# Kernel tuning notes

Measured on AMD Instinct MI355X. Metric: run time of the kernel, lower is better.

The kernel has to match this reference:

```python
import jax, jax.numpy as jnp
import numpy as np
from jax import lax

GS = 29          # grid_size
DW = 15          # displacement_width
DR = 0.4         # disp_range
N = GS ** 3      # 24389 control points
P = DW ** 2      # 225 in-plane displacements
WIN = (1, 1, 3, 3, 1)
ONE = (1, 1, 1, 1, 1)


def _axis(n):
    # align_corners=False pixel-center coords in [-1, 1], as torch affine_grid
    return (2.0 * jnp.arange(n, dtype=jnp.float32) + 1.0) / n - 1.0


def make_grids():
    a = _axis(GS)
    zc, yc, xc = jnp.meshgrid(a, a, a, indexing='ij')
    grid_xyz = jnp.stack([xc, yc, zc], -1).reshape(-1, 3)  # (N,3) xyz, d-major flatten
    s = DR * _axis(DW)
    A, B = jnp.meshgrid(s, s, indexing='ij')
    Z = jnp.zeros_like(A)
    sx = jnp.stack([B, A, Z], -1).reshape(-1, 3)  # z=0 plane: (s[w], s[h], 0)
    sy = jnp.stack([B, Z, A], -1).reshape(-1, 3)  # y=0 plane: (s[w], 0, s[d])
    sz = jnp.stack([Z, B, A], -1).reshape(-1, 3)  # x=0 plane: (0, s[h], s[d])
    shift_2d = jnp.stack([sx, sy, sz], axis=1)    # (P,3,3): [disp, plane, xyz]
    return grid_xyz, shift_2d


def trilerp(vol, coords, border):
    # vol (C,D,H,W); coords (...,3) normalized xyz; align_corners=False trilinear
    C, D, H, W = vol.shape
    vflat = vol.reshape(C, -1)
    x, y, z = coords[..., 0], coords[..., 1], coords[..., 2]
    ix = 0.5 * ((x + 1.0) * W - 1.0)
    iy = 0.5 * ((y + 1.0) * H - 1.0)
    iz = 0.5 * ((z + 1.0) * D - 1.0)
    x0 = jnp.floor(ix); y0 = jnp.floor(iy); z0 = jnp.floor(iz)
    fx, fy, fz = ix - x0, iy - y0, iz - z0
    x0 = x0.astype(jnp.int32); y0 = y0.astype(jnp.int32); z0 = z0.astype(jnp.int32)
    out = 0.0
    for dz in (0, 1):
        wz = fz if dz else 1.0 - fz
        zi = z0 + dz
        for dy in (0, 1):
            wy = fy if dy else 1.0 - fy
            yi = y0 + dy
            for dx in (0, 1):
                wx = fx if dx else 1.0 - fx
                xi = x0 + dx
                w = wx * wy * wz
                xc = jnp.clip(xi, 0, W - 1)
                yc = jnp.clip(yi, 0, H - 1)
                zc = jnp.clip(zi, 0, D - 1)
                if not border:  # padding_mode='zeros'
                    inb = ((xi >= 0) & (xi < W) & (yi >= 0) & (yi < H) & (zi >= 0) & (zi < D))
                    w = w * inb.astype(vol.dtype)
                idx = (zc * H + yc) * W + xc
                out = out + vflat[:, idx] * w
    return out  # (C, *coords.shape[:-1])


def pad_dh(x):
    # ReplicationPad3d((0,0,2,2,2,2)) on a 5D tensor: pad dims 2 and 3 by 2
    return jnp.pad(x, ((0, 0), (0, 0), (2, 2), (2, 2), (0, 0)), mode='edge')


def minpool(x):
    # -MaxPool3d((3,3,1))(-x)
    return -lax.reduce_window(-x, -jnp.inf, lax.max, WIN, ONE, 'VALID')


def avgpool(x):
    # AvgPool3d((3,3,1), stride=1)
    return lax.reduce_window(x, 0.0, lax.add, WIN, ONE, 'VALID') / 9.0


def grid_smooth(cost):
    # (1,N,DW,DW,3) -> two 3x3 avg passes over the 29^3 control grid (d,h axes)
    cp = cost.transpose(2, 3, 4, 0, 1).reshape(1, 3 * P, GS, GS, GS)
    cp = avgpool(avgpool(pad_dh(cp)))
    return cp.transpose(0, 2, 3, 4, 1).reshape(1, N, DW, DW, 3)


def setup_inputs() -> dict:
    key = jax.random.key(0)
    k1, k2 = jax.random.split(key)
    C, V = 8, 64
    feat00 = jax.random.normal(k1, (1, C, V, V, V), jnp.float32)
    feat50 = jax.random.normal(k2, (1, C, V, V, V), jnp.float32)
    grid_xyz, shift_2d = make_grids()
    shift_2d_min = jnp.array(jnp.broadcast_to(shift_2d[None, None], (1, N, P, 3, 3)))
    alpha = jnp.array([1.0, 0.1, 1.0, 1.0, 0.1, 5.0], jnp.float32)
    return {"feat00": feat00, "feat50": feat50, "shift_2d_min": shift_2d_min,
            "grid_xyz": grid_xyz, "shift_2d": shift_2d, "alpha": alpha}


def reference(feat00, feat50, shift_2d_min, grid_xyz, shift_2d, alpha):
    grid29 = grid_xyz.reshape(GS, GS * GS, 3)
    sm = shift_2d_min.reshape(GS, GS * GS, P, 3, 3)
    f00, f50 = feat00[0], feat50[0]

    def chunk(args):
        g, s = args                                                # (841,3), (841,P,3,3)
        mov = trilerp(f50, g[:, None, None, :] + s, border=True)   # (C,841,P,3)
        fix = trilerp(f00, g, border=False)                        # (C,841)
        ssd = jnp.sum((fix[:, :, None, None] - mov) ** 2, axis=0)  # (841,P,3)
        return alpha[1] + alpha[0] * ssd

    pdd = lax.map(chunk, (grid29, sm)).reshape(1, N, DW, DW, 3)
    cost = avgpool(minpool(pad_dh(pdd)))
    cost = alpha[4] + alpha[2] * pdd + alpha[3] * grid_smooth(cost)
    cost = avgpool(minpool(pad_dh(cost)))
    cost_avg = grid_smooth(cost).reshape(N, P, 3)
    cost_soft = jax.nn.softmax(-alpha[5] * cost_avg, axis=1)
    pred_xyz = 0.5 * jnp.einsum('npk,pkd->nd', cost_soft, shift_2d)
    return cost_soft.reshape(N, 1, DW, DW, 3), pred_xyz, cost_avg
```

## Files before the change

### kernel.cpp

```cpp
#include <hip/hip_runtime.h>
#include <math.h>

#define GS   29
#define GS2  841
#define NCP  24389
#define DW   15
#define PP   225
#define CH   675
#define CC   8
#define VV   64
#define V3   262144

typedef __attribute__((ext_vector_type(8))) _Float16 half8;

__device__ __forceinline__ float sv(int i) {
    return 0.4f * ((2.f * i + 1.f) * (1.f / 15.f) - 1.f);
}

__global__ __launch_bounds__(256) void make_vols(const float* __restrict__ in,
                                                 _Float16* __restrict__ volA,
                                                 _Float16* __restrict__ volB) {
    int v = blockIdx.x * 256 + threadIdx.x;
    if (v >= V3) return;
    int z = v >> 12, y = (v >> 6) & 63, x = v & 63;
    half8 h;
#pragma unroll
    for (int c = 0; c < CC; c++) h[c] = (_Float16)in[c * V3 + v];
    *(half8*)(volA + (size_t)v * 8) = h;
    *(half8*)(volB + (size_t)((((z << 6) | x) << 6) | y) * 8) = h;
}

__global__ __launch_bounds__(256) void pdd_pool_n(const float* __restrict__ f00,
                                                  const _Float16* __restrict__ volA,
                                                  const _Float16* __restrict__ volB,
                                                  const float* __restrict__ grid,
                                                  const float* __restrict__ alpha,
                                                  _Float16* __restrict__ pdd,
                                                  _Float16* __restrict__ pool) {
    int n = blockIdx.x;
    int tid = threadIdx.x;
    __shared__ __align__(16) _Float16 fixh[8];
    __shared__ float rowp[CH];
    __shared__ float smin[3 * 289];

    float gx = grid[n * 3 + 0], gy = grid[n * 3 + 1], gz = grid[n * 3 + 2];

    if (tid < 8) {
        float ix = 0.5f * ((gx + 1.f) * VV - 1.f);
        float iy = 0.5f * ((gy + 1.f) * VV - 1.f);
        float iz = 0.5f * ((gz + 1.f) * VV - 1.f);
        float x0f = floorf(ix), y0f = floorf(iy), z0f = floorf(iz);
        float fx = ix - x0f, fy = iy - y0f, fz = iz - z0f;
        int x0 = (int)x0f, y0 = (int)y0f, z0 = (int)z0f;
        const float* fc = f00 + tid * V3;
        float acc = 0.f;
        for (int dz = 0; dz < 2; dz++) {
            int zi = z0 + dz; float wz = dz ? fz : 1.f - fz;
            for (int dy = 0; dy < 2; dy++) {
                int yi = y0 + dy; float wy = dy ? fy : 1.f - fy;
                for (int dx = 0; dx < 2; dx++) {
                    int xi = x0 + dx; float wx = dx ? fx : 1.f - fx;
                    if (xi >= 0 && xi < VV && yi >= 0 && yi < VV && zi >= 0 && zi < VV)
                        acc += wx * wy * wz * fc[(zi * VV + yi) * VV + xi];
                }
            }
        }
        fixh[tid] = (_Float16)acc;
    }
    __syncthreads();

    if (tid < PP) {
        int p = tid;
        int h_ = p / 15, w_ = p - 15 * h_;
        float A = sv(h_), B = sv(w_);
        half8 f8 = *(const half8*)fixh;
        float a0 = alpha[0], a1 = alpha[1];

        for (int k = 0; k < 3; k++) {
            float pu, pv, pw;
            const _Float16* vol;
            if (k == 0)      { pu = gx + B; pv = gy + A; pw = gz;     vol = volA; }
            else if (k == 1) { pu = gx + B; pv = gy;     pw = gz + A; vol = volA; }
            else             { pu = gy + B; pv = gx;     pw = gz + A; vol = volB; }

            float iu = 0.5f * ((pu + 1.f) * VV - 1.f);
            float iv = 0.5f * ((pv + 1.f) * VV - 1.f);
            float iw = 0.5f * ((pw + 1.f) * VV - 1.f);
            float u0f = floorf(iu), v0f = floorf(iv), w0f = floorf(iw);
            float fu = iu - u0f, fv = iv - v0f, fw = iw - w0f;
            int u0 = (int)u0f, v0 = (int)v0f, w0 = (int)w0f;

            int p0 = min(max(u0, 0), VV - 2);
            float wAu = (u0 < 0) ? 1.f : ((u0 >= VV - 1) ? 0.f : (1.f - fu));
            float wBu = 1.f - wAu;
            int v0c = min(max(v0, 0), VV - 1), v1c = min(max(v0 + 1, 0), VV - 1);
            int w0c = min(max(w0, 0), VV - 1), w1c = min(max(w0 + 1, 0), VV - 1);
            float wv0 = 1.f - fv, wv1 = fv;
            float ww0 = 1.f - fw, ww1 = fw;

            half8 acc = {0, 0, 0, 0, 0, 0, 0, 0};
#define PAIR(WC, VC, WGT) {                                               \
                float fA_ = (WGT) * wAu, fB_ = (WGT) * wBu;               \
                _Float16 hA_ = (_Float16)fA_, hB_ = (_Float16)fB_;        \
                half8 hA8 = {hA_, hA_, hA_, hA_, hA_, hA_, hA_, hA_};     \
                half8 hB8 = {hB_, hB_, hB_, hB_, hB_, hB_, hB_, hB_};     \
                const _Float16* vp = vol + (size_t)((((WC) * VV) + (VC)) * VV + p0) * 8; \
                half8 lo = *(const half8*)vp;                             \
                half8 hi = *(const half8*)(vp + 8);                       \
                acc += hA8 * lo;                                          \
                acc += hB8 * hi;                                          \
            }
            PAIR(w0c, v0c, ww0 * wv0)
            PAIR(w0c, v1c, ww0 * wv1)
            PAIR(w1c, v0c, ww1 * wv0)
            PAIR(w1c, v1c, ww1 * wv1)
#undef PAIR

            half8 d8 = f8 - acc;
            float ssd = 0.f;
#pragma unroll
            for (int c = 0; c < 8; c++) { float dc = (float)d8[c]; ssd = fmaf(dc, dc, ssd); }
            rowp[p * 3 + k] = a1 + a0 * ssd;
        }
    }
    __syncthreads();

    for (int idx = tid; idx < 867; idx += 256) {
        int k = idx / 289; int r = idx - 289 * k; int a = r / 17; int b = r - 17 * a;
        float mn = 1e30f;
        for (int u = 0; u < 3; u++) {
            int hh = min(max(a + u - 2, 0), 14);
            for (int v = 0; v < 3; v++) {
                int ww = min(max(b + v - 2, 0), 14);
                mn = fminf(mn, rowp[(hh * 15 + ww) * 3 + k]);
            }
        }
        smin[idx] = mn;
    }
    __syncthreads();

    for (int i = tid; i < CH; i += 256) {
        pdd[(size_t)n * CH + i] = (_Float16)rowp[i];
        int p = i / 3, k = i - 3 * p;
        int h = p / 15, w = p - 15 * h;
        float acc = 0.f;
        for (int a = 0; a < 3; a++)
            for (int b = 0; b < 3; b++)
                acc += smin[k * 289 + (h + a) * 17 + (w + b)];
        pool[(size_t)n * CH + i] = (_Float16)(acc * (1.f / 9.f));
    }
}

__global__ __launch_bounds__(256) void gs_z2_h(const _Float16* __restrict__ in,
                                               _Float16* __restrict__ out) {
    const int ZS = GS2 * CH;
    int id = blockIdx.x * 256 + threadIdx.x;
    if (id >= ZS) return;
    const float w0 = 1.f / 9.f, w1 = 2.f / 9.f, w2 = 3.f / 9.f;
    const _Float16* p = in + id;
    float v0 = (float)p[0], v1 = v0, v2 = v0;
    float v3 = (float)p[ZS], v4 = (float)p[2 * (size_t)ZS];
    for (int z = 0; z < GS; z++) {
        out[id + (size_t)z * ZS] = (_Float16)(w0 * v0 + w1 * v1 + w2 * v2 + w1 * v3 + w0 * v4);
        v0 = v1; v1 = v2; v2 = v3; v3 = v4;
        int zn = z + 3; if (zn > GS - 1) zn = GS - 1;
        v4 = (float)p[(size_t)zn * ZS];
    }
}

__global__ __launch_bounds__(256) void gs_y_cost2_h(const _Float16* __restrict__ zt,
                                                    _Float16* pc,
                                                    const float* __restrict__ alpha) {
    const int ZS = GS2 * CH, YS = GS * CH;
    int id = blockIdx.x * 256 + threadIdx.x;
    if (id >= GS * YS) return;
    int z = id / YS; int rem = id - z * YS;
    size_t base = (size_t)z * ZS + rem;
    const float w0 = 1.f / 9.f, w1 = 2.f / 9.f, w2 = 3.f / 9.f;
    float a2 = alpha[2], a3 = alpha[3], a4 = alpha[4];
    const _Float16* p = zt + base;
    float v0 = (float)p[0], v1 = v0, v2 = v0;
    float v3 = (float)p[YS], v4 = (float)p[2 * (size_t)YS];
    for (int y = 0; y < GS; y++) {
        size_t idx = base + (size_t)y * YS;
        float acc = w0 * v0 + w1 * v1 + w2 * v2 + w1 * v3 + w0 * v4;
        float cur = (float)pc[idx];
        pc[idx] = (_Float16)(a4 + a2 * cur + a3 * acc);
        v0 = v1; v1 = v2; v2 = v3; v3 = v4;
        int yn = y + 3; if (yn > GS - 1) yn = GS - 1;
        v4 = (float)p[(size_t)yn * YS];
    }
}

__global__ __launch_bounds__(256) void gs_y2_hf(const _Float16* __restrict__ zt,
                                                float* __restrict__ out) {
    const int ZS = GS2 * CH, YS = GS * CH;
    int id = blockIdx.x * 256 + threadIdx.x;
    if (id >= GS * YS) return;
    int z = id / YS; int rem = id - z * YS;
    size_t base = (size_t)z * ZS + rem;
    const float w0 = 1.f / 9.f, w1 = 2.f / 9.f, w2 = 3.f / 9.f;
    const _Float16* p = zt + base;
    float v0 = (float)p[0], v1 = v0, v2 = v0;
    float v3 = (float)p[YS], v4 = (float)p[2 * (size_t)YS];
    for (int y = 0; y < GS; y++) {
        out[base + (size_t)y * YS] = w0 * v0 + w1 * v1 + w2 * v2 + w1 * v3 + w0 * v4;
        v0 = v1; v1 = v2; v2 = v3; v3 = v4;
        int yn = y + 3; if (yn > GS - 1) yn = GS - 1;
        v4 = (float)p[(size_t)yn * YS];
    }
}

__global__ __launch_bounds__(256) void pool_h(const _Float16* __restrict__ in,
                                              _Float16* __restrict__ out) {
    int n = blockIdx.x;
    int tid = threadIdx.x;
    __shared__ float sin_[CH];
    __shared__ float smn[17 * 17 * 3];
    for (int i = tid; i < CH; i += 256) sin_[i] = (float)in[(size_t)n * CH + i];
    __syncthreads();
    for (int idx = tid; idx < 17 * 17 * 3; idx += 256) {
        int a = idx / 51; int r = idx - 51 * a; int b = r / 3; int k = r - 3 * b;
        float mn = 1e30f;
        for (int u = 0; u < 3; u++) {
            int hh = min(max(a + u - 2, 0), 14);
            for (int v = 0; v < 3; v++) {
                int ww = min(max(b + v - 2, 0), 14);
                mn = fminf(mn, sin_[(hh * 15 + ww) * 3 + k]);
            }
        }
        smn[idx] = mn;
    }
    __syncthreads();
    for (int s = tid; s < CH; s += 256) {
        int h = s / 45; int r = s - 45 * h; int w = r / 3; int k = r - 3 * w;
        float acc = 0.f;
        for (int a = 0; a < 3; a++)
            for (int b = 0; b < 3; b++)
                acc += smn[(h + a) * 51 + (w + b) * 3 + k];
        out[(size_t)n * CH + s] = (_Float16)(acc * (1.f / 9.f));
    }
}

__global__ __launch_bounds__(256) void softmax_pred2(const float* __restrict__ ca,
                                                     const float* __restrict__ alpha,
                                                     float* __restrict__ soft,
                                                     float* __restrict__ pred) {
    int n = blockIdx.x;
    int tid = threadIdx.x;
    int wave = tid >> 6, lane = tid & 63;
    __shared__ float vals[CH];
    __shared__ float partial[3][3];
    for (int i = tid; i < CH; i += 256) vals[i] = ca[(size_t)n * CH + i];
    __syncthreads();
    float a5 = alpha[5];
    if (wave < 3) {
        int k = wave;
        float v[4], e[4];
        float m = -1e30f;
#pragma unroll
        for (int j = 0; j < 4; j++) {
            int p = lane + 64 * j;
            v[j] = (p < PP) ? -a5 * vals[p * 3 + k] : -1e30f;
            m = fmaxf(m, v[j]);
        }
#pragma unroll
        for (int o = 32; o > 0; o >>= 1) m = fmaxf(m, __shfl_xor(m, o));
        float sum = 0.f;
#pragma unroll
        for (int j = 0; j < 4; j++) {
            int p = lane + 64 * j;
            e[j] = (p < PP) ? __expf(v[j] - m) : 0.f;
            sum += e[j];
        }
#pragma unroll
        for (int o = 32; o > 0; o >>= 1) sum += __shfl_xor(sum, o);
        float inv = 1.f / sum;
        float px = 0.f, py = 0.f, pz = 0.f;
#pragma unroll
        for (int j = 0; j < 4; j++) {
            int p = lane + 64 * j;
            if (p < PP) {
                float s = e[j] * inv;
                vals[p * 3 + k] = s;
                int h_ = p / 15, w_ = p - 15 * h_;
                float A = sv(h_), B = sv(w_);
                if (k == 0)      { px += s * B; py += s * A; }
                else if (k == 1) { px += s * B; pz += s * A; }
                else             { py += s * B; pz += s * A; }
            }
        }
#pragma unroll
        for (int o = 32; o > 0; o >>= 1) {
            px += __shfl_xor(px, o);
            py += __shfl_xor(py, o);
            pz += __shfl_xor(pz, o);
        }
        if (lane == 0) { partial[k][0] = px; partial[k][1] = py; partial[k][2] = pz; }
    }
    __syncthreads();
    if (tid < 3) pred[(size_t)n * 3 + tid] = 0.5f * (partial[0][tid] + partial[1][tid] + partial[2][tid]);
    for (int i = tid; i < CH; i += 256) soft[(size_t)n * CH + i] = vals[i];
}

extern "C" void kernel_launch(void* const* d_in, const int* in_sizes, int n_in,
                              void* d_out, int out_size, void* d_ws, size_t ws_size,
                              hipStream_t stream) {
    const float* f00   = (const float*)d_in[0];
    const float* f50   = (const float*)d_in[1];
    const float* grid  = (const float*)d_in[3];
    const float* alpha = (const float*)d_in[5];

    float* out0 = (float*)d_out;
    float* out1 = out0 + (size_t)NCP * CH;
    float* out2 = out1 + (size_t)NCP * 3;

    char* ws = (char*)d_ws;
    _Float16* volA = (_Float16*)ws;
    _Float16* volB = volA + (size_t)V3 * 8;
    _Float16* H0 = volB + (size_t)V3 * 8;
    _Float16* H1 = H0 + (size_t)NCP * CH;
    _Float16* H2 = H1 + (size_t)NCP * CH;

    make_vols<<<(V3 + 255) / 256, 256, 0, stream>>>(f50, volA, volB);

    pdd_pool_n<<<NCP, 256, 0, stream>>>(f00, volA, volB, grid, alpha, H0, H1);

    const int TOT = GS2 * CH;
    const int gb2 = (TOT + 255) / 256;

    gs_z2_h<<<gb2, 256, 0, stream>>>(H1, H2);
    gs_y_cost2_h<<<gb2, 256, 0, stream>>>(H2, H0, alpha);

    pool_h<<<NCP, 256, 0, stream>>>(H0, H1);
    gs_z2_h<<<gb2, 256, 0, stream>>>(H1, H2);
    gs_y2_hf<<<gb2, 256, 0, stream>>>(H2, out2);

    softmax_pred2<<<NCP, 256, 0, stream>>>(out2, alpha, out0, out1);
}
```

Baseline: 558.9 us.

## Fuse separable grid smoothing into per-point pooling and softmax kernels

Replaces the separate z- and y-direction Gaussian smoothing passes with a direct 5x5 weighted gather over neighbouring control points. That gather is folded into the cost/min-avg pool kernel and into the softmax kernel, and the row stride is padded to 676 so half4 vector loads stay aligned. This cuts the number of kernel launches and the full-array intermediate round trips through global memory. In exchange, each point now reads 25 neighbour rows directly instead of running two streamed 1D passes, which adds redundant reads that rely on cache hits.

```diff
diff --git a/kernel.cpp b/kernel.cpp
--- a/kernel.cpp
+++ b/kernel.cpp
@@ -7,11 +7,13 @@
 #define DW   15
 #define PP   225
 #define CH   675
+#define CHP  676
 #define CC   8
 #define VV   64
 #define V3   262144
 
 typedef __attribute__((ext_vector_type(8))) _Float16 half8;
+typedef __attribute__((ext_vector_type(4))) _Float16 half4;
 
 __device__ __forceinline__ float sv(int i) {
     return 0.4f * ((2.f * i + 1.f) * (1.f / 15.f) - 1.f);
@@ -140,119 +142,133 @@
     __syncthreads();
 
     for (int i = tid; i < CH; i += 256) {
-        pdd[(size_t)n * CH + i] = (_Float16)rowp[i];
+        pdd[(size_t)n * CHP + i] = (_Float16)rowp[i];
         int p = i / 3, k = i - 3 * p;
         int h = p / 15, w = p - 15 * h;
         float acc = 0.f;
         for (int a = 0; a < 3; a++)
             for (int b = 0; b < 3; b++)
                 acc += smin[k * 289 + (h + a) * 17 + (w + b)];
-        pool[(size_t)n * CH + i] = (_Float16)(acc * (1.f / 9.f));
-    }
-}
-
-__global__ __launch_bounds__(256) void gs_z2_h(const _Float16* __restrict__ in,
-                                               _Float16* __restrict__ out) {
-    const int ZS = GS2 * CH;
-    int id = blockIdx.x * 256 + threadIdx.x;
-    if (id >= ZS) return;
-    const float w0 = 1.f / 9.f, w1 = 2.f / 9.f, w2 = 3.f / 9.f;
-    const _Float16* p = in + id;
-    float v0 = (float)p[0], v1 = v0, v2 = v0;
-    float v3 = (float)p[ZS], v4 = (float)p[2 * (size_t)ZS];
-    for (int z = 0; z < GS; z++) {
-        out[id + (size_t)z * ZS] = (_Float16)(w0 * v0 + w1 * v1 + w2 * v2 + w1 * v3 + w0 * v4);
-        v0 = v1; v1 = v2; v2 = v3; v3 = v4;
-        int zn = z + 3; if (zn > GS - 1) zn = GS - 1;
-        v4 = (float)p[(size_t)zn * ZS];
-    }
-}
-
-__global__ __launch_bounds__(256) void gs_y_cost2_h(const _Float16* __restrict__ zt,
-                                                    _Float16* pc,
-                                                    const float* __restrict__ alpha) {
-    const int ZS = GS2 * CH, YS = GS * CH;
-    int id = blockIdx.x * 256 + threadIdx.x;
-    if (id >= GS * YS) return;
-    int z = id / YS; int rem = id - z * YS;
-    size_t base = (size_t)z * ZS + rem;
-    const float w0 = 1.f / 9.f, w1 = 2.f / 9.f, w2 = 3.f / 9.f;
-    float a2 = alpha[2], a3 = alpha[3], a4 = alpha[4];
-    const _Float16* p = zt + base;
-    float v0 = (float)p[0], v1 = v0, v2 = v0;
-    float v3 = (float)p[YS], v4 = (float)p[2 * (size_t)YS];
-    for (int y = 0; y < GS; y++) {
-        size_t idx = base + (size_t)y * YS;
-        float acc = w0 * v0 + w1 * v1 + w2 * v2 + w1 * v3 + w0 * v4;
-        float cur = (float)pc[idx];
-        pc[idx] = (_Float16)(a4 + a2 * cur + a3 * acc);
-        v0 = v1; v1 = v2; v2 = v3; v3 = v4;
-        int yn = y + 3; if (yn > GS - 1) yn = GS - 1;
-        v4 = (float)p[(size_t)yn * YS];
-    }
-}
-
-__global__ __launch_bounds__(256) void gs_y2_hf(const _Float16* __restrict__ zt,
-                                                float* __restrict__ out) {
-    const int ZS = GS2 * CH, YS = GS * CH;
-    int id = blockIdx.x * 256 + threadIdx.x;
-    if (id >= GS * YS) return;
-    int z = id / YS; int rem = id - z * YS;
-    size_t base = (size_t)z * ZS + rem;
-    const float w0 = 1.f / 9.f, w1 = 2.f / 9.f, w2 = 3.f / 9.f;
-    const _Float16* p = zt + base;
-    float v0 = (float)p[0], v1 = v0, v2 = v0;
-    float v3 = (float)p[YS], v4 = (float)p[2 * (size_t)YS];
-    for (int y = 0; y < GS; y++) {
-        out[base + (size_t)y * YS] = w0 * v0 + w1 * v1 + w2 * v2 + w1 * v3 + w0 * v4;
-        v0 = v1; v1 = v2; v2 = v3; v3 = v4;
-        int yn = y + 3; if (yn > GS - 1) yn = GS - 1;
-        v4 = (float)p[(size_t)yn * YS];
-    }
-}
-
-__global__ __launch_bounds__(256) void pool_h(const _Float16* __restrict__ in,
-                                              _Float16* __restrict__ out) {
-    int n = blockIdx.x;
-    int tid = threadIdx.x;
-    __shared__ float sin_[CH];
+        pool[(size_t)n * CHP + i] = (_Float16)(acc * (1.f / 9.f));
+    }
+}
+
+__global__ __launch_bounds__(256) void cost_pool2(const _Float16* __restrict__ pool1,
+                                                  const _Float16* __restrict__ pdd,
+                                                  const float* __restrict__ alpha,
+                                                  _Float16* __restrict__ pool2) {
+    int n = blockIdx.x, tid = threadIdx.x;
+    int x = n % GS; int zy = n / GS; int y = zy % GS; int z = zy / GS;
+    __shared__ int   sbase[25];
+    __shared__ float swt[25];
+    __shared__ float rowp[CHP];
     __shared__ float smn[17 * 17 * 3];
-    for (int i = tid; i < CH; i += 256) sin_[i] = (float)in[(size_t)n * CH + i];
-    __syncthreads();
-    for (int idx = tid; idx < 17 * 17 * 3; idx += 256) {
-        int a = idx / 51; int r = idx - 51 * a; int b = r / 3; int k = r - 3 * b;
+
+    if (tid < 25) {
+        int dz = tid / 5, dy = tid - 5 * (tid / 5);
+        int zz = min(max(z + dz - 2, 0), GS - 1);
+        int yy = min(max(y + dy - 2, 0), GS - 1);
+        sbase[tid] = ((zz * GS + yy) * GS + x) * CHP;
+        float tz = 3.f - fabsf((float)dz - 2.f);
+        float ty = 3.f - fabsf((float)dy - 2.f);
+        swt[tid] = tz * ty * (1.f / 81.f);
+    }
+    __syncthreads();
+
+    if (tid < 169) {
+        int c0 = tid * 4;
+        float s0 = 0.f, s1 = 0.f, s2 = 0.f, s3 = 0.f;
+#pragma unroll
+        for (int t = 0; t < 25; t++) {
+            int off = sbase[t] + c0;
+            float w = swt[t];
+            half4 hv = *(const half4*)(pool1 + off);
+            s0 = fmaf(w, (float)hv[0], s0);
+            s1 = fmaf(w, (float)hv[1], s1);
+            s2 = fmaf(w, (float)hv[2], s2);
+            s3 = fmaf(w, (float)hv[3], s3);
+        }
+        float a2 = alpha[2], a3 = alpha[3], a4 = alpha[4];
+        half4 pv = *(const half4*)(pdd + (size_t)n * CHP + c0);
+        rowp[c0 + 0] = a4 + a2 * (float)pv[0] + a3 * s0;
+        rowp[c0 + 1] = a4 + a2 * (float)pv[1] + a3 * s1;
+        rowp[c0 + 2] = a4 + a2 * (float)pv[2] + a3 * s2;
+        rowp[c0 + 3] = a4 + a2 * (float)pv[3] + a3 * s3;
+    }
+    __syncthreads();
+
+    for (int idx = tid; idx < 867; idx += 256) {
+        int k = idx / 289; int r = idx - 289 * k; int a = r / 17; int b = r - 17 * a;
         float mn = 1e30f;
         for (int u = 0; u < 3; u++) {
             int hh = min(max(a + u - 2, 0), 14);
             for (int v = 0; v < 3; v++) {
                 int ww = min(max(b + v - 2, 0), 14);
-                mn = fminf(mn, sin_[(hh * 15 + ww) * 3 + k]);
+                mn = fminf(mn, rowp[(hh * 15 + ww) * 3 + k]);
             }
         }
         smn[idx] = mn;
     }
     __syncthreads();
-    for (int s = tid; s < CH; s += 256) {
-        int h = s / 45; int r = s - 45 * h; int w = r / 3; int k = r - 3 * w;
+
+    for (int i = tid; i < CH; i += 256) {
+        int p = i / 3, k = i - 3 * p;
+        int h = p / 15, w = p - 15 * h;
         float acc = 0.f;
         for (int a = 0; a < 3; a++)
             for (int b = 0; b < 3; b++)
-                acc += smn[(h + a) * 51 + (w + b) * 3 + k];
-        out[(size_t)n * CH + s] = (_Float16)(acc * (1.f / 9.f));
-    }
-}
-
-__global__ __launch_bounds__(256) void softmax_pred2(const float* __restrict__ ca,
-                                                     const float* __restrict__ alpha,
-                                                     float* __restrict__ soft,
-                                                     float* __restrict__ pred) {
-    int n = blockIdx.x;
-    int tid = threadIdx.x;
+                acc += smn[k * 289 + (h + a) * 17 + (w + b)];
+        pool2[(size_t)n * CHP + i] = (_Float16)(acc * (1.f / 9.f));
+    }
+}
+
+__global__ __launch_bounds__(256) void smooth_softmax(const _Float16* __restrict__ pool2,
+                                                      const float* __restrict__ alpha,
+                                                      float* __restrict__ ca,
+                                                      float* __restrict__ soft,
+                                                      float* __restrict__ pred) {
+    int n = blockIdx.x, tid = threadIdx.x;
+    int x = n % GS; int zy = n / GS; int y = zy % GS; int z = zy / GS;
     int wave = tid >> 6, lane = tid & 63;
-    __shared__ float vals[CH];
+    __shared__ int   sbase[25];
+    __shared__ float swt[25];
+    __shared__ float vals[CHP];
     __shared__ float partial[3][3];
-    for (int i = tid; i < CH; i += 256) vals[i] = ca[(size_t)n * CH + i];
-    __syncthreads();
+
+    if (tid < 25) {
+        int dz = tid / 5, dy = tid - 5 * (tid / 5);
+        int zz = min(max(z + dz - 2, 0), GS - 1);
+        int yy = min(max(y + dy - 2, 0), GS - 1);
+        sbase[tid] = ((zz * GS + yy) * GS + x) * CHP;
+        float tz = 3.f - fabsf((float)dz - 2.f);
+        float ty = 3.f - fabsf((float)dy - 2.f);
+        swt[tid] = tz * ty * (1.f / 81.f);
+    }
+    __syncthreads();
+
+    if (tid < 169) {
+        int c0 = tid * 4;
+        float s0 = 0.f, s1 = 0.f, s2 = 0.f, s3 = 0.f;
+#pragma unroll
+        for (int t = 0; t < 25; t++) {
+            int off = sbase[t] + c0;
+            float w = swt[t];
+            half4 hv = *(const half4*)(pool2 + off);
+            s0 = fmaf(w, (float)hv[0], s0);
+            s1 = fmaf(w, (float)hv[1], s1);
+            s2 = fmaf(w, (float)hv[2], s2);
+            s3 = fmaf(w, (float)hv[3], s3);
+        }
+        vals[c0 + 0] = s0;
+        vals[c0 + 1] = s1;
+        vals[c0 + 2] = s2;
+        vals[c0 + 3] = s3;
+    }
+    __syncthreads();
+
+    for (int i = tid; i < CH; i += 256) ca[(size_t)n * CH + i] = vals[i];
+    __syncthreads();
+
     float a5 = alpha[5];
     if (wave < 3) {
         int k = wave;
@@ -319,22 +335,14 @@
     _Float16* volA = (_Float16*)ws;
     _Float16* volB = volA + (size_t)V3 * 8;
     _Float16* H0 = volB + (size_t)V3 * 8;
-    _Float16* H1 = H0 + (size_t)NCP * CH;
-    _Float16* H2 = H1 + (size_t)NCP * CH;
+    _Float16* H1 = H0 + (size_t)NCP * CHP;
+    _Float16* H2 = H1 + (size_t)NCP * CHP;
 
     make_vols<<<(V3 + 255) / 256, 256, 0, stream>>>(f50, volA, volB);
 
     pdd_pool_n<<<NCP, 256, 0, stream>>>(f00, volA, volB, grid, alpha, H0, H1);
 
-    const int TOT = GS2 * CH;
-    const int gb2 = (TOT + 255) / 256;
-
-    gs_z2_h<<<gb2, 256, 0, stream>>>(H1, H2);
-    gs_y_cost2_h<<<gb2, 256, 0, stream>>>(H2, H0, alpha);
-
-    pool_h<<<NCP, 256, 0, stream>>>(H0, H1);
-    gs_z2_h<<<gb2, 256, 0, stream>>>(H1, H2);
-    gs_y2_hf<<<gb2, 256, 0, stream>>>(H2, out2);
-
-    softmax_pred2<<<NCP, 256, 0, stream>>>(out2, alpha, out0, out1);
-}
+    cost_pool2<<<NCP, 256, 0, stream>>>(H1, H0, alpha, H2);
+
+    smooth_softmax<<<NCP, 256, 0, stream>>>(H2, alpha, out2, out0, out1);
+}
```

After: 572.5 us. 2.4% more time.
